# Kernel tuning notes

Measured on AMD Instinct MI355X. Metric: run time of the kernel, lower is better.

## Reference

```python
import jax, jax.numpy as jnp
import numpy as np

NEG = -1e9  # finite stand-in for -inf (grad-safe)


def _ctc_forward_sum(logits, text_len, mel_len):
    """CTC forward (alpha) log-likelihood for one sample.

    logits: [T, C] raw attention scores (mel frames x text tokens).
    Target sequence is arange(text_len); blank index is 0 (matching
    torch.nn.CTCLoss defaults as used by ForwardSumLossWithBlank).
    Returns mean-reduced CTC loss (negative log-lik / target_length),
    with zero_infinity semantics.
    """
    T, C = logits.shape
    classes = jnp.arange(C)
    # log_softmax over only the valid text positions (original slices to text_len)
    lp = jax.nn.log_softmax(jnp.where(classes[None, :] < text_len, logits, NEG), axis=-1)  # [T, C]

    S = 2 * C + 1  # extended label length upper bound (blank-interleaved)
    s = jnp.arange(S)
    # extended labels: even positions -> blank (class 0), odd position s -> (s-1)//2
    ext_labels = jnp.where(s % 2 == 1, (s - 1) // 2, 0)
    lp_ext = lp[:, ext_labels]  # [T, S]
    # skip (s-2 -> s) transition allowed iff label(s) != blank and != label(s-2).
    # labels are arange so distinct; s=1 has label 0 == blank -> disallowed.
    skip_ok = (s % 2 == 1) & (s >= 3)

    alpha0 = jnp.full((S,), NEG, logits.dtype)
    alpha0 = alpha0.at[0].set(lp_ext[0, 0]).at[1].set(lp_ext[0, 1])

    def step(alpha, inp):
        t, lp_t = inp
        prev1 = jnp.concatenate([jnp.full((1,), NEG, alpha.dtype), alpha[:-1]])
        prev2 = jnp.concatenate([jnp.full((2,), NEG, alpha.dtype), alpha[:-2]])
        prev2 = jnp.where(skip_ok, prev2, NEG)
        new = jnp.logaddexp(jnp.logaddexp(alpha, prev1), prev2) + lp_t
        # freeze alpha past this sample's mel length
        return jnp.where(t < mel_len, new, alpha), None

    alpha, _ = jax.lax.scan(step, alpha0, (jnp.arange(1, T), lp_ext[1:]))

    s_end = 2 * text_len  # last valid extended position (final blank)
    ll = jnp.logaddexp(alpha[s_end], alpha[s_end - 1])
    loss = -ll / text_len.astype(logits.dtype)
    # zero_infinity=True: impossible alignments contribute 0
    return jnp.where(ll > NEG / 2, loss, jnp.zeros_like(loss))


def setup_inputs() -> dict:
    key = jax.random.key(0)
    k1, k2, k3 = jax.random.split(key, 3)
    B, T, C = 32, 2000, 400
    attn_logprob = jax.random.normal(k1, (B, 1, T, C), dtype=jnp.float32)
    text_lens = jax.random.randint(k2, (B,), 64, C + 1)
    mel_lens = jax.random.randint(k3, (B,), 1024, T + 1)
    return {"attn_logprob": attn_logprob, "text_lens": text_lens, "mel_lens": mel_lens}


def reference(attn_logprob, text_lens, mel_lens):
    logits = attn_logprob[:, 0]  # [B, T, C] (squeeze channel, matching permute in torch)
    losses = jax.vmap(_ctc_forward_sum)(logits, text_lens, mel_lens)
    return jnp.mean(losses)
```

## Files before the change

### kernel.cpp

```cpp
#include <hip/hip_runtime.h>


static constexpr int B_ = 32;
static constexpr int T_ = 2000;
static constexpr int C_ = 400;
static constexpr float M0f    = 1e20f;
static constexpr float LOGM0f = 46.05170186f;

typedef float f32x2 __attribute__((ext_vector_type(2)));
typedef float f32x8v __attribute__((ext_vector_type(8)));
struct __attribute__((packed, aligned(4))) f32x8u { f32x8v v; };

template <int CTRL>
__device__ __forceinline__ float dppmov(float v) {
    return __int_as_float(__builtin_amdgcn_update_dpp(
        0, __float_as_int(v), CTRL, 0xF, 0xF, true));
}

__device__ __forceinline__ float bcast0(float v) {
    return __int_as_float(__builtin_amdgcn_readfirstlane(__float_as_int(v)));
}

__device__ __forceinline__ unsigned bf16rne(float f) {
    unsigned u = __float_as_uint(f);
    u += 0x7FFFu + ((u >> 16) & 1u);
    return u >> 16;
}

__global__ __launch_bounds__(256) void k_prob(const float* __restrict__ logits,
                                              const int* __restrict__ text_lens,
                                              unsigned short* __restrict__ pbf,
                                              float* __restrict__ ls) {
    const int lane = threadIdx.x & 63;
    const int row  = blockIdx.x * 4 + (threadIdx.x >> 6);
    const int b    = row / T_;
    const int tl   = text_lens[b];
    const float* __restrict__ r = logits + (size_t)row * C_;

    const int c0 = lane * 8;
    float v[8];
    if (c0 < C_) {
        const float4 a = *(const float4*)(r + c0);
        const float4 c = *(const float4*)(r + c0 + 4);
        v[0]=a.x; v[1]=a.y; v[2]=a.z; v[3]=a.w; v[4]=c.x; v[5]=c.y; v[6]=c.z; v[7]=c.w;
    } else {
#pragma unroll
        for (int e = 0; e < 8; ++e) v[e] = 0.f;
    }
    float ex[8]; float s = 0.f;
#pragma unroll
    for (int e = 0; e < 8; ++e) {
        const int c = c0 + e;
        const float t = (c < tl) ? __expf(v[e]) : 0.f;
        ex[e] = t; s += t;
    }
#pragma unroll
    for (int off = 32; off; off >>= 1) s += __shfl_xor(s, off);

    if (pbf) {
        const float inv = 1.0f / s;
        uint4 st;
        st.x = bf16rne(ex[0]*inv) | (bf16rne(ex[4]*inv) << 16);
        st.y = bf16rne(ex[1]*inv) | (bf16rne(ex[5]*inv) << 16);
        st.z = bf16rne(ex[2]*inv) | (bf16rne(ex[6]*inv) << 16);
        st.w = bf16rne(ex[3]*inv) | (bf16rne(ex[7]*inv) << 16);
        *(uint4*)(pbf + (size_t)row * 512 + c0) = st;
        if (lane == 0) ls[row] = ex[0] * inv;
    } else {
        if (lane == 0) ls[row] = __logf(s);
    }
}

__global__ __launch_bounds__(256) void k_lsum(const float* __restrict__ ls,
                                              const int* __restrict__ mel_lens,
                                              float* __restrict__ lsums) {
    const int b  = blockIdx.x;
    const int ml = mel_lens[b];
    float s = 0.f;
    for (int i = threadIdx.x; i < ml; i += 256) s += ls[(size_t)b * T_ + i];
#pragma unroll
    for (int off = 32; off; off >>= 1) s += __shfl_xor(s, off);
    __shared__ float ws[4];
    if ((threadIdx.x & 63) == 0) ws[threadIdx.x >> 6] = s;
    __syncthreads();
    if (threadIdx.x == 0) lsums[b] = (ws[0] + ws[1]) + (ws[2] + ws[3]);
}

__device__ __forceinline__ void renorm_exp_pk(f32x2* __restrict__ Ae,
                                              f32x2* __restrict__ Ao, int& exacc) {
    const f32x2 m0 = __builtin_elementwise_max(__builtin_elementwise_max(Ae[0], Ao[0]),
                                               __builtin_elementwise_max(Ae[1], Ao[1]));
    const f32x2 m1 = __builtin_elementwise_max(__builtin_elementwise_max(Ae[2], Ao[2]),
                                               __builtin_elementwise_max(Ae[3], Ao[3]));
    const f32x2 m2 = __builtin_elementwise_max(m0, m1);
    float m = fmaxf(m2.x, m2.y);
    m = fmaxf(m, dppmov<0x111>(m));
    m = fmaxf(m, dppmov<0x112>(m));
    m = fmaxf(m, dppmov<0x114>(m));
    m = fmaxf(m, dppmov<0x118>(m));
    m = fmaxf(m, dppmov<0x142>(m));
    m = fmaxf(m, dppmov<0x143>(m));
    const int wmb = __builtin_amdgcn_readlane(__float_as_int(m), 63);
    int ex = ((wmb >> 23) & 0xFF) - 127;
    if (ex < -60) ex = -60;
    exacc += ex - 66;
    const float scale = __int_as_float((unsigned)(193 - ex) << 23);
    const f32x2 sc = {scale, scale};
#pragma unroll
    for (int j = 0; j < 4; ++j) { Ae[j] *= sc; Ao[j] *= sc; }
}

__device__ __forceinline__ void update_pk(const float p0,
                                          const f32x2 pk0, const f32x2 pk1,
                                          const f32x2 pk2, const f32x2 pk3,
                                          f32x2* __restrict__ Ae, f32x2* __restrict__ Ao) {
    const float bnd = dppmov<0x138>(Ao[3].y);
    f32x2 prev0; prev0.x = bnd; prev0.y = Ao[3].x;
    const f32x2 E0 = Ae[0] + prev0;
    const f32x2 E1 = Ae[1] + Ao[0];
    const f32x2 E2 = Ae[2] + Ao[1];
    const f32x2 E3 = Ae[3] + Ao[2];
    const f32x2 T0 = Ao[0] + E0;
    const f32x2 T1 = Ao[1] + E1;
    const f32x2 T2 = Ao[2] + E2;
    const f32x2 T3 = Ao[3] + E3;
    const f32x2 vp0 = {p0, p0};
    Ae[0] = E0 * vp0; Ae[1] = E1 * vp0; Ae[2] = E2 * vp0; Ae[3] = E3 * vp0;
    Ao[0] = T0 * pk0; Ao[1] = T1 * pk1; Ao[2] = T2 * pk2; Ao[3] = T3 * pk3;
}

__global__ __launch_bounds__(64) void k_ctc_bf16(const unsigned short* __restrict__ pbf,
                                                 const int* __restrict__ text_lens,
                                                 const int* __restrict__ mel_lens,
                                                 const float* __restrict__ p0arr,
                                                 float* __restrict__ losses) {
    const int b    = blockIdx.x;
    const int lane = threadIdx.x;
    const int tl   = text_lens[b];
    const int ml   = mel_lens[b];
    const char* __restrict__ base = (const char*)(pbf + (size_t)b * T_ * 512);
    const float* __restrict__ p0b = p0arr + (size_t)b * T_;
    const unsigned laneoff = (unsigned)lane * 16;

    uint4 raw[16];
#pragma unroll
    for (int s = 0; s < 16; ++s)
        raw[s] = *(const uint4*)(base + ((unsigned)(s + 1) << 10) + laneoff);

    f32x2 Ae[4], Ao[4];
#pragma unroll
    for (int j = 0; j < 4; ++j) { Ae[j] = (f32x2){0.f, 0.f}; Ao[j] = (f32x2){0.f, 0.f}; }
    {
        const float p00 = p0b[0] * 0x1p66f;
        if (lane == 0) { Ae[0].x = p00; Ao[0].x = p00; }
    }
    int exacc = -66;

    f32x8v p0lo = ((const f32x8u*)(p0b + 1))->v;
    f32x8v p0hi = ((const f32x8u*)(p0b + 9))->v;
#define P0AT(S) (((S) < 8) ? p0lo[(S) & 7] : p0hi[(S) & 7])

#define CVT8(SLOT, P)  { const uint4 w = raw[SLOT];                                   \
        P[0].x=__uint_as_float(w.x<<16); P[0].y=__uint_as_float(w.x&0xFFFF0000u);     \
        P[1].x=__uint_as_float(w.y<<16); P[1].y=__uint_as_float(w.y&0xFFFF0000u);     \
        P[2].x=__uint_as_float(w.z<<16); P[2].y=__uint_as_float(w.z&0xFFFF0000u);     \
        P[3].x=__uint_as_float(w.w<<16); P[3].y=__uint_as_float(w.w&0xFFFF0000u); }

    f32x2 pA[4], pB[4];
    CVT8(0, pA)

#define STEP_MAIN(S, PIN, POUT, CLAMPED)                                       \
    { unsigned tr = (unsigned)(tb + (S) + 16);                                 \
      if (CLAMPED) { if ((int)tr > ml - 1) tr = (unsigned)(ml - 1); }          \
      raw[S] = *(const uint4*)(base + (tr << 10) + laneoff); }                 \
    CVT8(((S) + 1) & 15, POUT)                                                 \
    update_pk(P0AT(S), PIN[0], PIN[1], PIN[2], PIN[3], Ae, Ao);                \
    if (((S) & 7) == 7) renorm_exp_pk(Ae, Ao, exacc);

#define BLOCK16(CLAMPED)                                                       \
    { const f32x8v nlo = ((const f32x8u*)(p0b + tb + 16))->v;                  \
      const f32x8v nhi = ((const f32x8u*)(p0b + tb + 24))->v;                  \
      STEP_MAIN(0,  pA, pB, CLAMPED)                                           \
      STEP_MAIN(1,  pB, pA, CLAMPED)                                           \
      STEP_MAIN(2,  pA, pB, CLAMPED)                                           \
      STEP_MAIN(3,  pB, pA, CLAMPED)                                           \
      STEP_MAIN(4,  pA, pB, CLAMPED)                                           \
      STEP_MAIN(5,  pB, pA, CLAMPED)                                           \
      STEP_MAIN(6,  pA, pB, CLAMPED)                                           \
      STEP_MAIN(7,  pB, pA, CLAMPED)                                           \
      STEP_MAIN(8,  pA, pB, CLAMPED)                                           \
      STEP_MAIN(9,  pB, pA, CLAMPED)                                           \
      STEP_MAIN(10, pA, pB, CLAMPED)                                           \
      STEP_MAIN(11, pB, pA, CLAMPED)                                           \
      STEP_MAIN(12, pA, pB, CLAMPED)                                           \
      STEP_MAIN(13, pB, pA, CLAMPED)                                           \
      STEP_MAIN(14, pA, pB, CLAMPED)                                           \
      STEP_MAIN(15, pB, pA, CLAMPED)                                           \
      p0lo = nlo; p0hi = nhi; }

    int tb = 1;
    for (; tb + 32 <= ml; tb += 16) {
        BLOCK16(0)
    }
    if (tb + 16 <= ml) {
        BLOCK16(1)
        tb += 16;
    }

#define STEP_TAIL(S, PIN, POUT)                                                \
    if (tb + (S) < ml) {                                                       \
        CVT8(((S) + 1) & 15, POUT)                                             \
        update_pk(P0AT(S), PIN[0], PIN[1], PIN[2], PIN[3], Ae, Ao);            \
    }
    STEP_TAIL(0,  pA, pB)
    STEP_TAIL(1,  pB, pA)
    STEP_TAIL(2,  pA, pB)
    STEP_TAIL(3,  pB, pA)
    STEP_TAIL(4,  pA, pB)
    STEP_TAIL(5,  pB, pA)
    STEP_TAIL(6,  pA, pB)
    STEP_TAIL(7,  pB, pA)
    STEP_TAIL(8,  pA, pB)
    STEP_TAIL(9,  pB, pA)
    STEP_TAIL(10, pA, pB)
    STEP_TAIL(11, pB, pA)
    STEP_TAIL(12, pA, pB)
    STEP_TAIL(13, pB, pA)
    STEP_TAIL(14, pA, pB)
    STEP_TAIL(15, pB, pA)
#undef STEP_TAIL
#undef BLOCK16
#undef STEP_MAIN
#undef CVT8
#undef P0AT

    float contrib = 0.f;
#pragma unroll
    for (int j = 0; j < 4; ++j) {
        const int kx = lane * 8 + j;
        const int ky = kx + 4;
        if (kx == tl)     contrib += Ae[j].x;
        if (kx == tl - 1) contrib += Ao[j].x;
        if (ky == tl)     contrib += Ae[j].y;
        if (ky == tl - 1) contrib += Ao[j].y;
    }
#pragma unroll
    for (int off = 32; off; off >>= 1) contrib += __shfl_xor(contrib, off);
    if (lane == 0) {
        float loss = 0.f;
        if (contrib > 0.f) {
            const float ll = __logf(contrib) + (float)exacc * 0.69314718056f;
            loss = -ll / (float)tl;
        }
        losses[b] = loss;
    }
}

template <int PP>
__device__ __forceinline__ void step_update(const float p0, const float* __restrict__ p,
                                            float* __restrict__ aeven, float* __restrict__ aodd) {
    float prev = dppmov<0x138>(aodd[PP - 1]);
#pragma unroll
    for (int j = 0; j < PP; ++j) {
        const float oldodd = aodd[j];
        const float e = aeven[j] + prev;
        aeven[j] = e * p0;
        aodd[j]  = (oldodd + e) * p[j];
        prev = oldodd;
    }
}

template <int PP>
__device__ __forceinline__ void renorm(float* __restrict__ aeven, float* __restrict__ aodd,
                                       float& lognorm) {
    float m = 0.f;
#pragma unroll
    for (int j = 0; j < PP; ++j) m = fmaxf(m, fmaxf(aeven[j], aodd[j]));
    m = fmaxf(m, dppmov<0x111>(m));
    m = fmaxf(m, dppmov<0x112>(m));
    m = fmaxf(m, dppmov<0x114>(m));
    m = fmaxf(m, dppmov<0x118>(m));
    m = fmaxf(m, dppmov<0x142>(m));
    m = fmaxf(m, dppmov<0x143>(m));
    const float wm  = __int_as_float(__builtin_amdgcn_readlane(__float_as_int(m), 63));
    const float inv = 1.0f / wm;
    lognorm += __logf(wm) - LOGM0f;
#pragma unroll
    for (int j = 0; j < PP; ++j) {
        aeven[j] = (aeven[j] * inv) * M0f;
        aodd[j]  = (aodd[j]  * inv) * M0f;
    }
}

template <int PP>
__device__ __forceinline__ void ctc_run_slow(const float* __restrict__ Lb, float lsum,
                                             int tl, int ml, float* __restrict__ loss_out) {
    const int lane = threadIdx.x;
    const int base = lane * PP;
    int   idx[PP];
    float mask[PP];
#pragma unroll
    for (int j = 0; j < PP; ++j) {
        const int k = base + j;
        idx[j]  = (k < C_) ? k : (C_ - 1);
        mask[j] = (k < tl) ? 1.f : 0.f;
    }
    float raw[8][PP];
#pragma unroll
    for (int s = 0; s < 8; ++s) {
        const float* __restrict__ rowp = Lb + (size_t)(s + 1) * C_;
#pragma unroll
        for (int j = 0; j < PP; ++j) raw[s][j] = rowp[idx[j]];
    }
    float aeven[PP], aodd[PP];
#pragma unroll
    for (int j = 0; j < PP; ++j) { aeven[j] = 0.f; aodd[j] = 0.f; }
    {
        const float a00 = __expf(Lb[0]) * M0f;
        if (lane == 0) { aeven[0] = a00; aodd[0] = a00; }
    }
    float lognorm = -LOGM0f;
    int tb = 1;
    for (; tb + 8 <= ml; tb += 8) {
#pragma unroll
        for (int s = 0; s < 8; ++s) {
            const int tt = tb + s;
            const float p0 = __expf(bcast0(raw[s][0]));
            float p[PP];
#pragma unroll
            for (int j = 0; j < PP; ++j) p[j] = __expf(raw[s][j]) * mask[j];
            { int tr = tt + 8; if (tr > ml - 1) tr = ml - 1;
              const float* __restrict__ rowp = Lb + (size_t)tr * C_;
#pragma unroll
              for (int j = 0; j < PP; ++j) raw[s][j] = rowp[idx[j]]; }
            step_update<PP>(p0, p, aeven, aodd);
            if (s == 7) renorm<PP>(aeven, aodd, lognorm);
        }
    }
#pragma unroll
    for (int s = 0; s < 8; ++s) {
        const int tt = tb + s;
        if (tt < ml) {
            const float p0 = __expf(bcast0(raw[s][0]));
            float p[PP];
#pragma unroll
            for (int j = 0; j < PP; ++j) p[j] = __expf(raw[s][j]) * mask[j];
            step_update<PP>(p0, p, aeven, aodd);
            if (s == 7) renorm<PP>(aeven, aodd, lognorm);
        }
    }
    float contrib = 0.f;
#pragma unroll
    for (int j = 0; j < PP; ++j) {
        const int k = base + j;
        if (k == tl)     contrib += aeven[j];
        if (k == tl - 1) contrib += aodd[j];
    }
#pragma unroll
    for (int off = 32; off; off >>= 1) contrib += __shfl_xor(contrib, off);
    if (lane == 0) {
        float loss = 0.f;
        if (contrib > 0.f) {
            const float ll = __logf(contrib) + lognorm - lsum;
            loss = -ll / (float)tl;
        }
        *loss_out = loss;
    }
}

__global__ __launch_bounds__(64) void k_ctc_slow(const float* __restrict__ logits,
                                                 const int* __restrict__ text_lens,
                                                 const int* __restrict__ mel_lens,
                                                 const float* __restrict__ lsums,
                                                 float* __restrict__ losses) {
    const int b  = blockIdx.x;
    const int tl = text_lens[b];
    const int ml = mel_lens[b];
    const float lsum = lsums[b];
    const float* Lb = logits + (size_t)b * T_ * C_;
    float* lo = losses + b;
    const int PP = (tl + 1 + 63) >> 6;
    switch (PP) {
        case 1: ctc_run_slow<1>(Lb, lsum, tl, ml, lo); break;
        case 2: ctc_run_slow<2>(Lb, lsum, tl, ml, lo); break;
        case 3: ctc_run_slow<3>(Lb, lsum, tl, ml, lo); break;
        case 4: ctc_run_slow<4>(Lb, lsum, tl, ml, lo); break;
        case 5: ctc_run_slow<5>(Lb, lsum, tl, ml, lo); break;
        case 6: ctc_run_slow<6>(Lb, lsum, tl, ml, lo); break;
        default: ctc_run_slow<7>(Lb, lsum, tl, ml, lo); break;
    }
}

__global__ __launch_bounds__(64) void k_final(const float* __restrict__ losses,
                                              float* __restrict__ out) {
    const int lane = threadIdx.x;
    float v = (lane < B_) ? losses[lane] : 0.f;
#pragma unroll
    for (int off = 32; off; off >>= 1) v += __shfl_xor(v, off);
    if (lane == 0) out[0] = v * (1.0f / B_);
}

extern "C" void kernel_launch(void* const* d_in, const int* in_sizes, int n_in,
                              void* d_out, int out_size, void* d_ws, size_t ws_size,
                              hipStream_t stream) {
    const float* logits    = (const float*)d_in[0];
    const int*   text_lens = (const int*)d_in[1];
    const int*   mel_lens  = (const int*)d_in[2];
    float* out = (float*)d_out;

    const size_t PBF_BYTES  = (size_t)B_ * T_ * 512 * 2;
    const size_t tail_bytes = (size_t)B_ * T_ * 4 + 2 * B_ * 4 + 64;

    if (ws_size >= PBF_BYTES + tail_bytes) {
        unsigned short* pbf = (unsigned short*)d_ws;
        float* ls     = (float*)((char*)d_ws + PBF_BYTES);
        float* lsums  = ls + (size_t)B_ * T_;
        float* losses = lsums + B_;
        k_prob<<<B_ * T_ / 4, 256, 0, stream>>>(logits, text_lens, pbf, ls);
        k_ctc_bf16<<<B_, 64, 0, stream>>>(pbf, text_lens, mel_lens, ls, losses);
        k_final<<<1, 64, 0, stream>>>(losses, out);
    } else {
        float* ls     = (float*)d_ws;
        float* lsums  = ls + (size_t)B_ * T_;
        float* losses = lsums + B_;
        k_prob<<<B_ * T_ / 4, 256, 0, stream>>>(logits, text_lens, nullptr, ls);
        k_lsum<<<B_, 256, 0, stream>>>(ls, mel_lens, lsums);
        k_ctc_slow<<<B_, 64, 0, stream>>>(logits, text_lens, mel_lens, lsums, losses);
        k_final<<<1, 64, 0, stream>>>(losses, out);
    }
}
```

Measured before the change: 180.3 us.

## Split CTC alpha recursion across two wavefronts with LDS boundary ring handoff

Each batch sample's CTC forward recursion now runs on two wavefronts instead of one. Each wave owns half the extended-label positions, so it holds half as many alpha registers and does half the per-step arithmetic. Wave 0 writes its boundary alpha and exponent into an LDS ring every step and publishes progress through a shared flag, and wave 1 spins on that flag and injects the rescaled boundary value. The bf16 packing order in the probability kernel is changed to match the new per-wave data layout. The cost is spin-wait synchronisation, ldexp rescaling on every step, and a pipeline lag between the two waves, which could offset the shorter per-step critical path.

```diff
diff --git a/kernel.cpp b/kernel.cpp
--- a/kernel.cpp
+++ b/kernel.cpp
@@ -60,10 +60,10 @@
     if (pbf) {
         const float inv = 1.0f / s;
         uint4 st;
-        st.x = bf16rne(ex[0]*inv) | (bf16rne(ex[4]*inv) << 16);
-        st.y = bf16rne(ex[1]*inv) | (bf16rne(ex[5]*inv) << 16);
-        st.z = bf16rne(ex[2]*inv) | (bf16rne(ex[6]*inv) << 16);
-        st.w = bf16rne(ex[3]*inv) | (bf16rne(ex[7]*inv) << 16);
+        st.x = bf16rne(ex[0]*inv) | (bf16rne(ex[2]*inv) << 16);
+        st.y = bf16rne(ex[1]*inv) | (bf16rne(ex[3]*inv) << 16);
+        st.z = bf16rne(ex[4]*inv) | (bf16rne(ex[6]*inv) << 16);
+        st.w = bf16rne(ex[5]*inv) | (bf16rne(ex[7]*inv) << 16);
         *(uint4*)(pbf + (size_t)row * 512 + c0) = st;
         if (lane == 0) ls[row] = ex[0] * inv;
     } else {
@@ -86,13 +86,27 @@
     if (threadIdx.x == 0) lsums[b] = (ws[0] + ws[1]) + (ws[2] + ws[3]);
 }
 
-__device__ __forceinline__ void renorm_exp_pk(f32x2* __restrict__ Ae,
-                                              f32x2* __restrict__ Ao, int& exacc) {
-    const f32x2 m0 = __builtin_elementwise_max(__builtin_elementwise_max(Ae[0], Ao[0]),
+template <int W>
+__device__ __forceinline__ void update_pk2(const float p0, const f32x2 pk0, const f32x2 pk1,
+                                           f32x2* __restrict__ Ae, f32x2* __restrict__ Ao,
+                                           const float inj, const float mask0) {
+    float bx = dppmov<0x138>(Ao[1].y);
+    if constexpr (W == 1) bx = fmaf(inj, mask0, bx);
+    f32x2 prev0; prev0.x = bx; prev0.y = Ao[1].x;
+    const f32x2 E0 = Ae[0] + prev0;
+    const f32x2 E1 = Ae[1] + Ao[0];
+    const f32x2 T0 = Ao[0] + E0;
+    const f32x2 T1 = Ao[1] + E1;
+    const f32x2 vp0 = {p0, p0};
+    Ae[0] = E0 * vp0; Ae[1] = E1 * vp0;
+    Ao[0] = T0 * pk0; Ao[1] = T1 * pk1;
+}
+
+template <int W>
+__device__ __forceinline__ void renorm2(f32x2* __restrict__ Ae, f32x2* __restrict__ Ao,
+                                        int& exacc, const int exl) {
+    const f32x2 m2 = __builtin_elementwise_max(__builtin_elementwise_max(Ae[0], Ao[0]),
                                                __builtin_elementwise_max(Ae[1], Ao[1]));
-    const f32x2 m1 = __builtin_elementwise_max(__builtin_elementwise_max(Ae[2], Ao[2]),
-                                               __builtin_elementwise_max(Ae[3], Ao[3]));
-    const f32x2 m2 = __builtin_elementwise_max(m0, m1);
     float m = fmaxf(m2.x, m2.y);
     m = fmaxf(m, dppmov<0x111>(m));
     m = fmaxf(m, dppmov<0x112>(m));
@@ -101,104 +115,101 @@
     m = fmaxf(m, dppmov<0x142>(m));
     m = fmaxf(m, dppmov<0x143>(m));
     const int wmb = __builtin_amdgcn_readlane(__float_as_int(m), 63);
+    if constexpr (W == 1) {
+        if (wmb == 0) { exacc = __builtin_amdgcn_readfirstlane(exl); return; }
+    }
     int ex = ((wmb >> 23) & 0xFF) - 127;
     if (ex < -60) ex = -60;
     exacc += ex - 66;
     const float scale = __int_as_float((unsigned)(193 - ex) << 23);
     const f32x2 sc = {scale, scale};
-#pragma unroll
-    for (int j = 0; j < 4; ++j) { Ae[j] *= sc; Ao[j] *= sc; }
-}
-
-__device__ __forceinline__ void update_pk(const float p0,
-                                          const f32x2 pk0, const f32x2 pk1,
-                                          const f32x2 pk2, const f32x2 pk3,
-                                          f32x2* __restrict__ Ae, f32x2* __restrict__ Ao) {
-    const float bnd = dppmov<0x138>(Ao[3].y);
-    f32x2 prev0; prev0.x = bnd; prev0.y = Ao[3].x;
-    const f32x2 E0 = Ae[0] + prev0;
-    const f32x2 E1 = Ae[1] + Ao[0];
-    const f32x2 E2 = Ae[2] + Ao[1];
-    const f32x2 E3 = Ae[3] + Ao[2];
-    const f32x2 T0 = Ao[0] + E0;
-    const f32x2 T1 = Ao[1] + E1;
-    const f32x2 T2 = Ao[2] + E2;
-    const f32x2 T3 = Ao[3] + E3;
-    const f32x2 vp0 = {p0, p0};
-    Ae[0] = E0 * vp0; Ae[1] = E1 * vp0; Ae[2] = E2 * vp0; Ae[3] = E3 * vp0;
-    Ao[0] = T0 * pk0; Ao[1] = T1 * pk1; Ao[2] = T2 * pk2; Ao[3] = T3 * pk3;
-}
-
-__global__ __launch_bounds__(64) void k_ctc_bf16(const unsigned short* __restrict__ pbf,
-                                                 const int* __restrict__ text_lens,
-                                                 const int* __restrict__ mel_lens,
-                                                 const float* __restrict__ p0arr,
-                                                 float* __restrict__ losses) {
-    const int b    = blockIdx.x;
-    const int lane = threadIdx.x;
-    const int tl   = text_lens[b];
-    const int ml   = mel_lens[b];
-    const char* __restrict__ base = (const char*)(pbf + (size_t)b * T_ * 512);
-    const float* __restrict__ p0b = p0arr + (size_t)b * T_;
-    const unsigned laneoff = (unsigned)lane * 16;
-
-    uint4 raw[16];
+    Ae[0] *= sc; Ae[1] *= sc; Ao[0] *= sc; Ao[1] *= sc;
+}
+
+#define CVT4(SLOT, P)  { const uint2 wv = raw[SLOT];                                  \
+        P[0].x=__uint_as_float(wv.x<<16); P[0].y=__uint_as_float(wv.x&0xFFFF0000u);   \
+        P[1].x=__uint_as_float(wv.y<<16); P[1].y=__uint_as_float(wv.y&0xFFFF0000u); }
+
+template <int W>
+__device__ void ctc_half(const char* __restrict__ baseW, const float* __restrict__ p0b,
+                         int tl, int ml, uint2* __restrict__ ring_, volatile int* vflag,
+                         float* __restrict__ cs, int* __restrict__ es, int lane) {
+    const unsigned laneoff = (unsigned)lane * 8;
+
+    uint2 raw[16];
 #pragma unroll
     for (int s = 0; s < 16; ++s)
-        raw[s] = *(const uint4*)(base + ((unsigned)(s + 1) << 10) + laneoff);
-
-    f32x2 Ae[4], Ao[4];
-#pragma unroll
-    for (int j = 0; j < 4; ++j) { Ae[j] = (f32x2){0.f, 0.f}; Ao[j] = (f32x2){0.f, 0.f}; }
-    {
+        raw[s] = *(const uint2*)(baseW + ((unsigned)(s + 1) << 10) + laneoff);
+
+    f32x2 Ae[2], Ao[2];
+    Ae[0] = Ae[1] = Ao[0] = Ao[1] = (f32x2){0.f, 0.f};
+    if (W == 0 && lane == 0) {
         const float p00 = p0b[0] * 0x1p66f;
-        if (lane == 0) { Ae[0].x = p00; Ao[0].x = p00; }
+        Ae[0].x = p00; Ao[0].x = p00;
     }
     int exacc = -66;
+    int exl   = -66;
+    const float mask0 = (W == 1 && lane == 0) ? 1.f : 0.f;
 
     f32x8v p0lo = ((const f32x8u*)(p0b + 1))->v;
     f32x8v p0hi = ((const f32x8u*)(p0b + 9))->v;
 #define P0AT(S) (((S) < 8) ? p0lo[(S) & 7] : p0hi[(S) & 7])
 
-#define CVT8(SLOT, P)  { const uint4 w = raw[SLOT];                                   \
-        P[0].x=__uint_as_float(w.x<<16); P[0].y=__uint_as_float(w.x&0xFFFF0000u);     \
-        P[1].x=__uint_as_float(w.y<<16); P[1].y=__uint_as_float(w.y&0xFFFF0000u);     \
-        P[2].x=__uint_as_float(w.z<<16); P[2].y=__uint_as_float(w.z&0xFFFF0000u);     \
-        P[3].x=__uint_as_float(w.w<<16); P[3].y=__uint_as_float(w.w&0xFFFF0000u); }
-
-    f32x2 pA[4], pB[4];
-    CVT8(0, pA)
-
-#define STEP_MAIN(S, PIN, POUT, CLAMPED)                                       \
-    { unsigned tr = (unsigned)(tb + (S) + 16);                                 \
-      if (CLAMPED) { if ((int)tr > ml - 1) tr = (unsigned)(ml - 1); }          \
-      raw[S] = *(const uint4*)(base + (tr << 10) + laneoff); }                 \
-    CVT8(((S) + 1) & 15, POUT)                                                 \
-    update_pk(P0AT(S), PIN[0], PIN[1], PIN[2], PIN[3], Ae, Ao);                \
-    if (((S) & 7) == 7) renorm_exp_pk(Ae, Ao, exacc);
-
-#define BLOCK16(CLAMPED)                                                       \
-    { const f32x8v nlo = ((const f32x8u*)(p0b + tb + 16))->v;                  \
-      const f32x8v nhi = ((const f32x8u*)(p0b + tb + 24))->v;                  \
-      STEP_MAIN(0,  pA, pB, CLAMPED)                                           \
-      STEP_MAIN(1,  pB, pA, CLAMPED)                                           \
-      STEP_MAIN(2,  pA, pB, CLAMPED)                                           \
-      STEP_MAIN(3,  pB, pA, CLAMPED)                                           \
-      STEP_MAIN(4,  pA, pB, CLAMPED)                                           \
-      STEP_MAIN(5,  pB, pA, CLAMPED)                                           \
-      STEP_MAIN(6,  pA, pB, CLAMPED)                                           \
-      STEP_MAIN(7,  pB, pA, CLAMPED)                                           \
-      STEP_MAIN(8,  pA, pB, CLAMPED)                                           \
-      STEP_MAIN(9,  pB, pA, CLAMPED)                                           \
-      STEP_MAIN(10, pA, pB, CLAMPED)                                           \
-      STEP_MAIN(11, pB, pA, CLAMPED)                                           \
-      STEP_MAIN(12, pA, pB, CLAMPED)                                           \
-      STEP_MAIN(13, pB, pA, CLAMPED)                                           \
-      STEP_MAIN(14, pA, pB, CLAMPED)                                           \
-      STEP_MAIN(15, pB, pA, CLAMPED)                                           \
+    f32x2 pA[2], pB[2];
+    uint2 erA = {0u, 0u}, erB = {0u, 0u};
+    CVT4(0, pA)
+
+    int tb = 1;
+    if constexpr (W == 1) {
+        while (*vflag < 17) __builtin_amdgcn_s_sleep(1);
+        __threadfence_block();
+        erB = ring_[0];
+        erA = ring_[1];
+    }
+
+#define STEP2(S, PIN, POUT, CLAMPED)                                            \
+    {                                                                           \
+        { unsigned tr = (unsigned)(tb + (S) + 16);                              \
+          if (CLAMPED) { if ((int)tr > ml - 1) tr = (unsigned)(ml - 1); }       \
+          raw[S] = *(const uint2*)(baseW + (tr << 10) + laneoff); }             \
+        CVT4(((S) + 1) & 15, POUT)                                              \
+        float inj = 0.f;                                                        \
+        if constexpr (W == 1) {                                                 \
+            constexpr int Pr = ((S) ^ 1) & 1;                                   \
+            const uint2 e = Pr ? erB : erA;                                     \
+            inj = ldexpf(__uint_as_float(e.x), (int)e.y - exacc);               \
+            exl = (int)e.y;                                                     \
+            (Pr ? erB : erA) = ring_[tb + (S) + 1];                             \
+        }                                                                       \
+        update_pk2<W>(P0AT(S), PIN[0], PIN[1], Ae, Ao, inj, mask0);             \
+        if constexpr (W == 0) {                                                 \
+            uint2 pkv; pkv.x = __float_as_uint(Ao[1].y); pkv.y = (unsigned)exacc; \
+            ring_[(lane == 63) ? (tb + (S)) : 2040] = pkv;                      \
+        }                                                                       \
+        if (((S) & 7) == 7) renorm2<W>(Ae, Ao, exacc, exl);                     \
+    }
+
+#define BLOCK16(CLAMPED)                                                        \
+    { const f32x8v nlo = ((const f32x8u*)(p0b + tb + 16))->v;                   \
+      const f32x8v nhi = ((const f32x8u*)(p0b + tb + 24))->v;                   \
+      if constexpr (W == 1) {                                                   \
+          while (*vflag < tb + 16) __builtin_amdgcn_s_sleep(1);                 \
+          __threadfence_block();                                                \
+      }                                                                         \
+      STEP2(0,  pA, pB, CLAMPED)  STEP2(1,  pB, pA, CLAMPED)                    \
+      STEP2(2,  pA, pB, CLAMPED)  STEP2(3,  pB, pA, CLAMPED)                    \
+      STEP2(4,  pA, pB, CLAMPED)  STEP2(5,  pB, pA, CLAMPED)                    \
+      STEP2(6,  pA, pB, CLAMPED)  STEP2(7,  pB, pA, CLAMPED)                    \
+      STEP2(8,  pA, pB, CLAMPED)  STEP2(9,  pB, pA, CLAMPED)                    \
+      STEP2(10, pA, pB, CLAMPED)  STEP2(11, pB, pA, CLAMPED)                    \
+      STEP2(12, pA, pB, CLAMPED)  STEP2(13, pB, pA, CLAMPED)                    \
+      STEP2(14, pA, pB, CLAMPED)  STEP2(15, pB, pA, CLAMPED)                    \
+      if constexpr (W == 0) {                                                   \
+          __threadfence_block();                                                \
+          if (lane == 0) *vflag = tb + 15;                                      \
+      }                                                                         \
       p0lo = nlo; p0hi = nhi; }
 
-    int tb = 1;
     for (; tb + 32 <= ml; tb += 16) {
         BLOCK16(0)
     }
@@ -207,49 +218,104 @@
         tb += 16;
     }
 
-#define STEP_TAIL(S, PIN, POUT)                                                \
-    if (tb + (S) < ml) {                                                       \
-        CVT8(((S) + 1) & 15, POUT)                                             \
-        update_pk(P0AT(S), PIN[0], PIN[1], PIN[2], PIN[3], Ae, Ao);            \
-    }
-    STEP_TAIL(0,  pA, pB)
-    STEP_TAIL(1,  pB, pA)
-    STEP_TAIL(2,  pA, pB)
-    STEP_TAIL(3,  pB, pA)
-    STEP_TAIL(4,  pA, pB)
-    STEP_TAIL(5,  pB, pA)
-    STEP_TAIL(6,  pA, pB)
-    STEP_TAIL(7,  pB, pA)
-    STEP_TAIL(8,  pA, pB)
-    STEP_TAIL(9,  pB, pA)
-    STEP_TAIL(10, pA, pB)
-    STEP_TAIL(11, pB, pA)
-    STEP_TAIL(12, pA, pB)
-    STEP_TAIL(13, pB, pA)
-    STEP_TAIL(14, pA, pB)
-    STEP_TAIL(15, pB, pA)
-#undef STEP_TAIL
+    if constexpr (W == 1) {
+        while (*vflag < (1 << 29)) __builtin_amdgcn_s_sleep(1);
+        __threadfence_block();
+    }
+
+#define STEP_TAIL2(S, PIN, POUT)                                                \
+    if (tb + (S) < ml) {                                                        \
+        CVT4(((S) + 1) & 15, POUT)                                              \
+        float inj = 0.f;                                                        \
+        if constexpr (W == 1) {                                                 \
+            constexpr int Pr = ((S) ^ 1) & 1;                                   \
+            const uint2 e = Pr ? erB : erA;                                     \
+            inj = ldexpf(__uint_as_float(e.x), (int)e.y - exacc);               \
+            (Pr ? erB : erA) = ring_[tb + (S) + 1];                             \
+        }                                                                       \
+        update_pk2<W>(P0AT(S), PIN[0], PIN[1], Ae, Ao, inj, mask0);             \
+        if constexpr (W == 0) {                                                 \
+            uint2 pkv; pkv.x = __float_as_uint(Ao[1].y); pkv.y = (unsigned)exacc; \
+            ring_[(lane == 63) ? (tb + (S)) : 2040] = pkv;                      \
+        }                                                                       \
+    }
+    STEP_TAIL2(0,  pA, pB)  STEP_TAIL2(1,  pB, pA)
+    STEP_TAIL2(2,  pA, pB)  STEP_TAIL2(3,  pB, pA)
+    STEP_TAIL2(4,  pA, pB)  STEP_TAIL2(5,  pB, pA)
+    STEP_TAIL2(6,  pA, pB)  STEP_TAIL2(7,  pB, pA)
+    STEP_TAIL2(8,  pA, pB)  STEP_TAIL2(9,  pB, pA)
+    STEP_TAIL2(10, pA, pB)  STEP_TAIL2(11, pB, pA)
+    STEP_TAIL2(12, pA, pB)  STEP_TAIL2(13, pB, pA)
+    STEP_TAIL2(14, pA, pB)  STEP_TAIL2(15, pB, pA)
+#undef STEP_TAIL2
 #undef BLOCK16
-#undef STEP_MAIN
-#undef CVT8
+#undef STEP2
 #undef P0AT
 
+    if constexpr (W == 0) {
+        __threadfence_block();
+        if (lane == 0) *vflag = (1 << 30);
+    }
+
     float contrib = 0.f;
-#pragma unroll
-    for (int j = 0; j < 4; ++j) {
-        const int kx = lane * 8 + j;
-        const int ky = kx + 4;
-        if (kx == tl)     contrib += Ae[j].x;
-        if (kx == tl - 1) contrib += Ao[j].x;
-        if (ky == tl)     contrib += Ae[j].y;
-        if (ky == tl - 1) contrib += Ao[j].y;
-    }
+    const int q0 = 256 * W + lane * 4;
+    if (q0     == tl)     contrib += Ae[0].x;
+    if (q0     == tl - 1) contrib += Ao[0].x;
+    if (q0 + 2 == tl)     contrib += Ae[0].y;
+    if (q0 + 2 == tl - 1) contrib += Ao[0].y;
+    if (q0 + 1 == tl)     contrib += Ae[1].x;
+    if (q0 + 1 == tl - 1) contrib += Ao[1].x;
+    if (q0 + 3 == tl)     contrib += Ae[1].y;
+    if (q0 + 3 == tl - 1) contrib += Ao[1].y;
 #pragma unroll
     for (int off = 32; off; off >>= 1) contrib += __shfl_xor(contrib, off);
-    if (lane == 0) {
+    if (lane == 0) { cs[W] = contrib; es[W] = exacc; }
+}
+
+__global__ __launch_bounds__(128) void k_ctc2(const unsigned short* __restrict__ pbf,
+                                              const int* __restrict__ text_lens,
+                                              const int* __restrict__ mel_lens,
+                                              const float* __restrict__ p0arr,
+                                              float* __restrict__ losses) {
+    __shared__ uint2 ring_[2048];
+    __shared__ int   flag_;
+    __shared__ float cs[2];
+    __shared__ int   es[2];
+    const int b    = blockIdx.x;
+    const int tid  = threadIdx.x;
+    const int w    = tid >> 6;
+    const int lane = tid & 63;
+    const int tl   = text_lens[b];
+    const int ml   = mel_lens[b];
+    if (tid == 0) {
+        flag_ = 0;
+        ring_[0].x = 0u; ring_[0].y = (unsigned)(-66);
+    }
+    __syncthreads();
+
+    const char* baseW = (const char*)(pbf + (size_t)b * T_ * 512) + 512 * w;
+    const float* p0b  = p0arr + (size_t)b * T_;
+    if (w == 0) ctc_half<0>(baseW, p0b, tl, ml, ring_, &flag_, cs, es, lane);
+    else        ctc_half<1>(baseW, p0b, tl, ml, ring_, &flag_, cs, es, lane);
+    __syncthreads();
+
+    if (tid == 0) {
+        const float c0 = cs[0], c1 = cs[1];
+        const bool h0 = c0 > 0.f, h1 = c1 > 0.f;
         float loss = 0.f;
-        if (contrib > 0.f) {
-            const float ll = __logf(contrib) + (float)exacc * 0.69314718056f;
+        if (h0 || h1) {
+            const float LN2 = 0.69314718056f;
+            float ll;
+            if (h0 && h1) {
+                const float l0 = __logf(c0) + (float)es[0] * LN2;
+                const float l1 = __logf(c1) + (float)es[1] * LN2;
+                const float M = fmaxf(l0, l1);
+                ll = M + __logf(__expf(l0 - M) + __expf(l1 - M));
+            } else if (h0) {
+                ll = __logf(c0) + (float)es[0] * LN2;
+            } else {
+                ll = __logf(c1) + (float)es[1] * LN2;
+            }
             loss = -ll / (float)tl;
         }
         losses[b] = loss;
@@ -417,7 +483,7 @@
         float* lsums  = ls + (size_t)B_ * T_;
         float* losses = lsums + B_;
         k_prob<<<B_ * T_ / 4, 256, 0, stream>>>(logits, text_lens, pbf, ls);
-        k_ctc_bf16<<<B_, 64, 0, stream>>>(pbf, text_lens, mel_lens, ls, losses);
+        k_ctc2<<<B_, 128, 0, stream>>>(pbf, text_lens, mel_lens, ls, losses);
         k_final<<<1, 64, 0, stream>>>(losses, out);
     } else {
         float* ls     = (float*)d_ws;
```

Measured after the change: 164.2 us. 1.1x faster.
